# Kernel tuning notes

Measured on AMD Instinct MI355X. Metric: run time of the kernel, lower is better.

## Reference

```python
import jax, jax.numpy as jnp
import numpy as np

B, N, NT, ET = 16, 38, 9, 4
NE = N * (N - 1) // 2          # 703 edge-generation steps
R = N + NE                     # repeat_num = 741 masked subgraphs
H = D = 128                    # nhid / nout
L = 12                         # num_flow_layer
EDIM = ET - 1                  # 3 relation types used by RGCN
EPS = 1e-5
TEMP = 0.1                     # straight-through argmax temperature


def _st_dis(x, w1, b1, w2, b2):
    # MLP -> logits -> straight-through one-hot(argmax)
    h = jnp.tanh(x @ w1.T + b1)
    logits = h @ w2.T + b2
    soft = jax.nn.softmax(logits / TEMP, axis=-1)
    hard = jax.nn.one_hot(jnp.argmax(logits, axis=-1), logits.shape[-1], dtype=logits.dtype)
    return soft + jax.lax.stop_gradient(hard - soft)


def _one_hot_add(inputs, shift):
    # (inputs + shift) mod vocab in one-hot space == circular conv via FFT
    out = jnp.fft.ifft(jnp.fft.fft(inputs, axis=-1) * jnp.fft.fft(shift, axis=-1), axis=-1)
    return jnp.real(out).astype(inputs.dtype)


def _gconv(x, adj, w):
    # x: (b, n, f_in), adj: (b, e, n, n), w: (e*f_out, f_in)
    b, n, _ = x.shape
    s = (x @ w.T).reshape(b, n, EDIM, -1)            # (b, n, e, f_out)
    return jnp.einsum('beij,bjeo->bio', adj, s)      # aggregate over relations


def _rgcn(x, adj, emb_w, gc1_w, gc2_w, gc3_w):
    h = x @ emb_w.T
    h = jax.nn.relu(_gconv(h, adj, gc1_w))
    h = jax.nn.relu(_gconv(h, adj, gc2_w))
    return _gconv(h, adj, gc3_w)                     # no relu on last layer


def setup_inputs():
    key = jax.random.key(0)
    ks = jax.random.split(key, 16)
    s = 0.1
    iu, ju = np.triu_indices(N, k=1)                 # canonical edge order (703, 2)
    return {
        'x': jax.random.uniform(ks[0], (B, N, NT), dtype=jnp.float32),
        'adj': jax.random.uniform(ks[1], (B, ET, N, N), dtype=jnp.float32),
        'x_deq': jax.random.normal(ks[2], (B, N, NT), dtype=jnp.float32),
        'adj_deq': jax.random.normal(ks[3], (B, NE, ET), dtype=jnp.float32),
        'mask_node': jax.random.uniform(ks[4], (R, N)) < 0.5,
        'mask_edge': jax.random.uniform(ks[5], (R, N, N)) < 0.5,
        'index_select_edge': jnp.asarray(np.stack([iu, ju], 1), dtype=jnp.int32),
        'emb_w': jax.random.normal(ks[6], (NT, NT), jnp.float32) * s,
        'gc1_w': jax.random.normal(ks[7], (EDIM * H, NT), jnp.float32) * s,
        'gc2_w': jax.random.normal(ks[8], (EDIM * H, H), jnp.float32) * s,
        'gc3_w': jax.random.normal(ks[9], (EDIM * D, H), jnp.float32) * s,
        'bn_gamma': jnp.ones((D,), jnp.float32),
        'bn_beta': jnp.zeros((D,), jnp.float32),
        'node_w1': jax.random.normal(ks[10], (L, H, D), jnp.float32) * s,
        'node_b1': jnp.zeros((L, H), jnp.float32),
        'node_w2': jax.random.normal(ks[11], (L, NT, H), jnp.float32) * s,
        'node_b2': jnp.zeros((L, NT), jnp.float32),
        'edge_w1': jax.random.normal(ks[12], (L, H, 3 * D), jnp.float32) * s,
        'edge_b1': jnp.zeros((L, H), jnp.float32),
        'edge_w2': jax.random.normal(ks[13], (L, ET, H), jnp.float32) * s,
        'edge_b2': jnp.zeros((L, ET), jnp.float32),
    }


def reference(x, adj, x_deq, adj_deq, mask_node, mask_edge, index_select_edge,
              emb_w, gc1_w, gc2_w, gc3_w, bn_gamma, bn_beta,
              node_w1, node_b1, node_w2, node_b2,
              edge_w1, edge_b1, edge_w2, edge_b2):
    adj3 = adj[:, :EDIM]                                              # (B,3,N,N)
    xr = jnp.where(mask_node[None, :, :, None], x[:, None], 0.0)      # (B,R,N,NT)
    ar = jnp.where(mask_edge[None, :, None], adj3[:, None], 0.0)      # (B,R,3,N,N)
    xr = xr.reshape(B * R, N, NT)
    ar = ar.reshape(B * R, EDIM, N, N)
    node_emb = _rgcn(xr, ar, emb_w, gc1_w, gc2_w, gc3_w)              # (B*R,N,D)
    # BatchNorm1d over channels (training-mode batch statistics, biased var)
    m = node_emb.mean(axis=(0, 1))
    v = node_emb.var(axis=(0, 1))
    node_emb = (node_emb - m) * jax.lax.rsqrt(v + EPS) * bn_gamma + bn_beta
    node_emb = node_emb.reshape(B, R, N, D)
    graph_emb = node_emb.sum(axis=2)                                  # (B,R,D)
    graph_emb_node = graph_emb[:, :N]                                 # (B,N,D)
    graph_emb_edge = graph_emb[:, N:, None]                           # (B,NE,1,D)
    all_node_emb_edge = node_emb[:, N:]                               # (B,NE,N,D)
    idx = jnp.broadcast_to(index_select_edge[None, :, :, None].astype(jnp.int32), (B, NE, 2, D))
    sel = jnp.take_along_axis(all_node_emb_edge, idx, axis=2)         # (B,NE,2,D)
    graph_node_emb_edge = jnp.concatenate([sel, graph_emb_edge], axis=2).reshape(B, NE, 3 * D)
    xd, ad = x_deq, adj_deq
    for i in range(L):
        nt = _st_dis(graph_emb_node, node_w1[i], node_b1[i], node_w2[i], node_b2[i]).astype(x.dtype)
        xd = _one_hot_add(xd, nt)
        et = _st_dis(graph_node_emb_edge, edge_w1[i], edge_b1[i], edge_w2[i], edge_b2[i]).astype(adj.dtype)
        ad = _one_hot_add(ad, et)
    return (xd, ad)
```

## Files before the change

### kernel.cpp

```cpp
#include <hip/hip_runtime.h>

#define B_   16
#define N_   38
#define NT_  9
#define ET_  4
#define NE_  703
#define R_   741
#define L_   12
#define BR_  11856

__global__ __launch_bounds__(128) void k_sx(const float* __restrict__ x,
                                            const float* __restrict__ emb_w,
                                            const float* __restrict__ gc1_w,
                                            float* __restrict__ sx)
{
  int bn = blockIdx.x;
  int t  = threadIdx.x;
  __shared__ float xr[NT_];
  __shared__ float hx[NT_];
  if (t < NT_) xr[t] = x[bn*NT_ + t];
  __syncthreads();
  if (t < NT_) {
    float s = 0.f;
    #pragma unroll
    for (int u = 0; u < NT_; ++u) s += xr[u] * emb_w[t*NT_ + u];
    hx[t] = s;
  }
  __syncthreads();
  for (int eo = t; eo < 384; eo += 128) {
    float s = 0.f;
    #pragma unroll
    for (int u = 0; u < NT_; ++u) s += hx[u] * gc1_w[eo*NT_ + u];
    sx[bn*384 + eo] = s;
  }
}

__global__ __launch_bounds__(128) void k_wt(const float* __restrict__ gc2_w,
                                            const float* __restrict__ gc3_w,
                                            float* __restrict__ Wt)
{
  int blk   = blockIdx.x;
  int which = blk / 384;
  int rem   = blk - which*384;
  int e     = rem >> 7;
  int k     = rem & 127;
  int o     = threadIdx.x;
  const float* src = which ? gc3_w : gc2_w;
  Wt[(((which*3 + e) << 7) + k)*128 + o] = src[((e << 7) + o)*128 + k];
}

__device__ __forceinline__ void fma4(float4& d, float a, const float4& s) {
  d.x += a*s.x; d.y += a*s.y; d.z += a*s.z; d.w += a*s.w;
}

__device__ __forceinline__ void ldA(const float* __restrict__ adj,
                                    const int* __restrict__ mask_edge,
                                    int b, int r, int e, int tid,
                                    float av[5], float a1v[2])
{
  #pragma unroll
  for (int t = 0; t < 5; ++t) {
    int m = tid + (t << 8);
    float v = 0.f;
    if (m < 1216) {
      int j = m >> 5, slot = m & 31;
      int i = (slot >> 2) + ((slot & 3) << 3);
      int   msk = mask_edge[(r*N_ + i)*N_ + j];
      float a   = adj[((b*ET_ + e)*N_ + i)*N_ + j];
      v = msk ? a : 0.f;
    }
    av[t] = v;
  }
  #pragma unroll
  for (int t = 0; t < 2; ++t) {
    int m = tid + (t << 8);
    float v = 0.f;
    if (m < 304) {
      int j = m >> 3;
      int i = (m & 7) + 32;
      if (i < N_) {
        int   msk = mask_edge[(r*N_ + i)*N_ + j];
        float a   = adj[((b*ET_ + e)*N_ + i)*N_ + j];
        v = msk ? a : 0.f;
      }
    }
    a1v[t] = v;
  }
}

__device__ __forceinline__ void stA(float* __restrict__ A4e,
                                    float* __restrict__ A1e, int tid,
                                    const float av[5], const float a1v[2])
{
  #pragma unroll
  for (int t = 0; t < 5; ++t) {
    int m = tid + (t << 8);
    if (m < 1216) A4e[m] = av[t];
  }
  #pragma unroll
  for (int t = 0; t < 2; ++t) {
    int m = tid + (t << 8);
    if (m < 304) A1e[m] = a1v[t];
  }
}

__device__ __forceinline__ void eacc_m(const float* __restrict__ A4e,
                                       const float* __restrict__ A1e,
                                       const float* __restrict__ S_l,
                                       int p, int c,
                                       const int* __restrict__ mn,
                                       float4 d[5])
{
  #pragma unroll 2
  for (int j = 0; j < 38; ++j) {
    if (!mn[j]) continue;
    float4 s4 = *(const float4*)&S_l[(j << 7) + (c << 2)];
    float4 a4 = *(const float4*)&A4e[(j << 5) + (p << 2)];
    float  a1 = A1e[(j << 3) + p];
    fma4(d[0], a4.x, s4); fma4(d[1], a4.y, s4); fma4(d[2], a4.z, s4);
    fma4(d[3], a4.w, s4); fma4(d[4], a1,   s4);
  }
}

__device__ __forceinline__ void eacc_u(const float* __restrict__ A4e,
                                       const float* __restrict__ A1e,
                                       const float* __restrict__ S_l,
                                       int p, int c,
                                       float4 d[5])
{
  #pragma unroll 4
  for (int j = 0; j < 38; ++j) {
    float4 s4 = *(const float4*)&S_l[(j << 7) + (c << 2)];
    float4 a4 = *(const float4*)&A4e[(j << 5) + (p << 2)];
    float  a1 = A1e[(j << 3) + p];
    fma4(d[0], a4.x, s4); fma4(d[1], a4.y, s4); fma4(d[2], a4.z, s4);
    fma4(d[3], a4.w, s4); fma4(d[4], a1,   s4);
  }
}

__device__ __forceinline__ void gemm_fused(const float* __restrict__ H_l,
                                           const float* __restrict__ Wb,
                                           int p, int c, float4 g[3][5])
{
  #pragma unroll
  for (int e = 0; e < 3; ++e)
    #pragma unroll
    for (int q = 0; q < 5; ++q) { g[e][q].x = 0.f; g[e][q].y = 0.f; g[e][q].z = 0.f; g[e][q].w = 0.f; }
  #pragma unroll 1
  for (int k0 = 0; k0 < 128; k0 += 4) {
    float4 h0 = *(const float4*)&H_l[((p+ 0) << 7) + k0];
    float4 h1 = *(const float4*)&H_l[((p+ 8) << 7) + k0];
    float4 h2 = *(const float4*)&H_l[((p+16) << 7) + k0];
    float4 h3 = *(const float4*)&H_l[((p+24) << 7) + k0];
    float4 h4 = *(const float4*)&H_l[((p+32) << 7) + k0];
    #pragma unroll
    for (int e = 0; e < 3; ++e) {
      const float* We = &Wb[(e << 14) + (k0 << 7) + (c << 2)];
      float4 w0 = *(const float4*)&We[  0];
      float4 w1 = *(const float4*)&We[128];
      float4 w2 = *(const float4*)&We[256];
      float4 w3 = *(const float4*)&We[384];
      fma4(g[e][0], h0.x, w0); fma4(g[e][0], h0.y, w1); fma4(g[e][0], h0.z, w2); fma4(g[e][0], h0.w, w3);
      fma4(g[e][1], h1.x, w0); fma4(g[e][1], h1.y, w1); fma4(g[e][1], h1.z, w2); fma4(g[e][1], h1.w, w3);
      fma4(g[e][2], h2.x, w0); fma4(g[e][2], h2.y, w1); fma4(g[e][2], h2.z, w2); fma4(g[e][2], h2.w, w3);
      fma4(g[e][3], h3.x, w0); fma4(g[e][3], h3.y, w1); fma4(g[e][3], h3.z, w2); fma4(g[e][3], h3.w, w3);
      fma4(g[e][4], h4.x, w0); fma4(g[e][4], h4.y, w1); fma4(g[e][4], h4.z, w2); fma4(g[e][4], h4.w, w3);
    }
  }
}

__device__ __forceinline__ void relu_store(float* __restrict__ H_l, int p, int c,
                                           const float4 d[5])
{
  #pragma unroll
  for (int q = 0; q < 5; ++q) {
    float4 t;
    t.x = fmaxf(d[q].x, 0.f); t.y = fmaxf(d[q].y, 0.f);
    t.z = fmaxf(d[q].z, 0.f); t.w = fmaxf(d[q].w, 0.f);
    *(float4*)&H_l[((p + (q << 3)) << 7) + (c << 2)] = t;
  }
}

__global__ __launch_bounds__(256) void k_rgcn(
    const float* __restrict__ adj, const int* __restrict__ mask_node,
    const int* __restrict__ mask_edge, const int* __restrict__ isel,
    const float* __restrict__ sx, const float* __restrict__ Wt,
    float* __restrict__ sumE, float* __restrict__ sumSq,
    float* __restrict__ selw)
{
  const int br  = blockIdx.x;
  const int b   = br / R_;
  const int r   = br - b*R_;
  const int tid = threadIdx.x;
  const int c   = tid & 31;
  const int p   = tid >> 5;

  __shared__ __align__(16) float A4_l[3*1216];
  __shared__ __align__(16) float A1_l[3*304];
  __shared__ __align__(16) float SH_l[40*128];
  __shared__ int mn_l[40];

  if (tid < 40) mn_l[tid] = (tid < 38) ? mask_node[r*N_ + tid] : 0;

  float av[5], a1v[2];
  ldA(adj, mask_edge, b, r, 0, tid, av, a1v);
  __syncthreads();

  float4 d[5];
  #pragma unroll
  for (int q = 0; q < 5; ++q) { d[q].x = d[q].y = d[q].z = d[q].w = 0.f; }

  for (int e = 0; e < 3; ++e) {
    for (int idx = tid; idx < 40*32; idx += 256) {
      int j = idx >> 5, q4 = idx & 31;
      float4 v; v.x = v.y = v.z = v.w = 0.f;
      if (j < N_ && mn_l[j]) v = *(const float4*)&sx[(b*N_ + j)*384 + (e << 7) + (q4 << 2)];
      *(float4*)&SH_l[(j << 7) + (q4 << 2)] = v;
    }
    stA(&A4_l[e*1216], &A1_l[e*304], tid, av, a1v);
    __syncthreads();
    if (e < 2) ldA(adj, mask_edge, b, r, e+1, tid, av, a1v);
    eacc_m(&A4_l[e*1216], &A1_l[e*304], SH_l, p, c, mn_l, d);
    __syncthreads();
  }
  relu_store(SH_l, p, c, d);
  __syncthreads();

  for (int gv = 0; gv < 2; ++gv) {
    float4 g[3][5];
    gemm_fused(SH_l, &Wt[gv*49152], p, c, g);
    #pragma unroll
    for (int q = 0; q < 5; ++q) { d[q].x = d[q].y = d[q].z = d[q].w = 0.f; }
    #pragma unroll
    for (int e = 0; e < 3; ++e) {
      __syncthreads();
      #pragma unroll
      for (int q = 0; q < 5; ++q)
        *(float4*)&SH_l[((p + (q << 3)) << 7) + (c << 2)] = g[e][q];
      __syncthreads();
      eacc_u(&A4_l[e*1216], &A1_l[e*304], SH_l, p, c, d);
    }
    if (gv == 0) {
      __syncthreads();
      relu_store(SH_l, p, c, d);
      __syncthreads();
    }
  }
  __syncthreads();

  {
    float4 sA, sB;
    sA.x = d[0].x+d[1].x+d[2].x+d[3].x+d[4].x;
    sA.y = d[0].y+d[1].y+d[2].y+d[3].y+d[4].y;
    sA.z = d[0].z+d[1].z+d[2].z+d[3].z+d[4].z;
    sA.w = d[0].w+d[1].w+d[2].w+d[3].w+d[4].w;
    sB.x = d[0].x*d[0].x+d[1].x*d[1].x+d[2].x*d[2].x+d[3].x*d[3].x+d[4].x*d[4].x;
    sB.y = d[0].y*d[0].y+d[1].y*d[1].y+d[2].y*d[2].y+d[3].y*d[3].y+d[4].y*d[4].y;
    sB.z = d[0].z*d[0].z+d[1].z*d[1].z+d[2].z*d[2].z+d[3].z*d[3].z+d[4].z*d[4].z;
    sB.w = d[0].w*d[0].w+d[1].w*d[1].w+d[2].w*d[2].w+d[3].w*d[3].w+d[4].w*d[4].w;
    *(float4*)&SH_l[( p      << 7) + (c << 2)] = sA;
    *(float4*)&SH_l[((8 + p) << 7) + (c << 2)] = sB;
  }
  __syncthreads();
  {
    int o = tid & 127, half = tid >> 7;
    float t = 0.f;
    #pragma unroll
    for (int pp = 0; pp < 8; ++pp) t += SH_l[(((half << 3) + pp) << 7) + o];
    if (half == 0) sumE [br*128 + o] = t;
    else           sumSq[br*128 + o] = t;
  }
  if (r >= N_) {
    int k  = r - N_;
    int iu = isel[2*k], ju = isel[2*k+1];
    if (p == (iu & 7)) {
      int mu = iu >> 3;
      float4 v = d[0];
      if (mu == 1) v = d[1]; else if (mu == 2) v = d[2];
      else if (mu == 3) v = d[3]; else if (mu == 4) v = d[4];
      *(float4*)&selw[(((b*NE_ + k)*2 + 0) << 7) + (c << 2)] = v;
    }
    if (p == (ju & 7)) {
      int mu = ju >> 3;
      float4 v = d[0];
      if (mu == 1) v = d[1]; else if (mu == 2) v = d[2];
      else if (mu == 3) v = d[3]; else if (mu == 4) v = d[4];
      *(float4*)&selw[(((b*NE_ + k)*2 + 1) << 7) + (c << 2)] = v;
    }
  }
}

__global__ __launch_bounds__(256) void k_bn1(const float* __restrict__ sumE,
                                             const float* __restrict__ sumSq,
                                             double* __restrict__ part)
{
  int g = blockIdx.x;
  int t = threadIdx.x;
  int o = t & 127, h = t >> 7;
  int lo = g*47;
  int hi = lo + 47; if (hi > BR_) hi = BR_;
  double a1 = 0.0, a2 = 0.0;
  for (int i = lo + h; i < hi; i += 2) {
    a1 += (double)sumE [i*128 + o];
    a2 += (double)sumSq[i*128 + o];
  }
  __shared__ double sh1[256], sh2[256];
  sh1[t] = a1; sh2[t] = a2;
  __syncthreads();
  if (h == 0) {
    part[g*128 + o]           = sh1[o] + sh1[128 + o];
    part[256*128 + g*128 + o] = sh2[o] + sh2[128 + o];
  }
}

__global__ __launch_bounds__(128) void k_bn2(const double* __restrict__ part,
                                             const float* __restrict__ gamma,
                                             const float* __restrict__ beta,
                                             float* __restrict__ bnsc,
                                             float* __restrict__ bnsh)
{
  int o = threadIdx.x;
  double s1 = 0.0, s2 = 0.0;
  for (int g = 0; g < 256; ++g) {
    s1 += part[g*128 + o];
    s2 += part[256*128 + g*128 + o];
  }
  double cnt = (double)BR_ * 38.0;
  double m   = s1 / cnt;
  double var = s2 / cnt - m*m;
  double rs  = 1.0 / sqrt(var + 1e-5);
  double sc  = (double)gamma[o] * rs;
  bnsc[o] = (float)sc;
  bnsh[o] = beta[o] - (float)(m * sc);
}

__global__ __launch_bounds__(128) void k_node(
    const float* __restrict__ sumE, const float* __restrict__ bnsc,
    const float* __restrict__ bnsh,
    const float* __restrict__ w1, const float* __restrict__ b1,
    const float* __restrict__ w2, const float* __restrict__ b2,
    const float* __restrict__ x_deq, float* __restrict__ out)
{
  int blk = blockIdx.x;
  int b   = blk / N_;
  int o   = threadIdx.x;
  __shared__ __align__(16) float xv[128];
  __shared__ __align__(16) float hb[128];
  __shared__ float lg[NT_];
  __shared__ int   P_s;
  int br = b*R_ + (blk - b*N_);
  xv[o] = sumE[br*128 + o]*bnsc[o] + 38.f*bnsh[o];
  if (o == 0) P_s = 0;
  __syncthreads();
  for (int l = 0; l < L_; ++l) {
    const float* wr = &w1[(l*128 + o)*128];
    float s = b1[l*128 + o];
    for (int k = 0; k < 128; k += 4) {
      float4 w4 = *(const float4*)&wr[k];
      s += w4.x*xv[k] + w4.y*xv[k+1] + w4.z*xv[k+2] + w4.w*xv[k+3];
    }
    hb[o] = tanhf(s);
    __syncthreads();
    if (o < NT_) {
      const float* w2r = &w2[(l*NT_ + o)*128];
      float s2 = b2[l*NT_ + o];
      for (int k = 0; k < 128; ++k) s2 += w2r[k]*hb[k];
      lg[o] = s2;
    }
    __syncthreads();
    if (o == 0) {
      int best = 0; float bv = lg[0];
      #pragma unroll
      for (int cc = 1; cc < NT_; ++cc) if (lg[cc] > bv) { bv = lg[cc]; best = cc; }
      P_s += best;
    }
    __syncthreads();
  }
  int P = P_s % NT_;
  if (o < NT_) {
    int srcc = o - P; if (srcc < 0) srcc += NT_;
    out[blk*NT_ + o] = x_deq[blk*NT_ + srcc];
  }
}

__global__ __launch_bounds__(256) void k_edge(
    const float* __restrict__ sumE, const float* __restrict__ selw,
    const float* __restrict__ bnsc, const float* __restrict__ bnsh,
    const float* __restrict__ w1, const float* __restrict__ b1,
    const float* __restrict__ w2, const float* __restrict__ b2,
    const float* __restrict__ adj_deq, float* __restrict__ out)
{
  int k = blockIdx.x;
  int t = threadIdx.x;
  int o = t & 127, g = t >> 7;
  __shared__ __align__(16) float xv[16][384];
  __shared__ __align__(16) float hb[16][132];
  __shared__ float lg[16][4];
  __shared__ int   Pf[16];

  for (int idx = t; idx < 16*128; idx += 256) {
    int b = idx >> 7, oo = idx & 127;
    float sc = bnsc[oo], sh = bnsh[oo];
    int base = ((b*NE_ + k)*2)*128;
    xv[b][oo]       = selw[base + oo]      *sc + sh;
    xv[b][128 + oo] = selw[base + 128 + oo]*sc + sh;
    xv[b][256 + oo] = sumE[(b*R_ + N_ + k)*128 + oo]*sc + 38.f*sh;
  }
  int Preg = 0;
  __syncthreads();

  for (int l = 0; l < L_; ++l) {
    float acc[8];
    #pragma unroll
    for (int bb = 0; bb < 8; ++bb) acc[bb] = b1[l*128 + o];
    const float* wr = &w1[(l*128 + o)*384];
    for (int kk = 0; kk < 384; kk += 4) {
      float4 w4 = *(const float4*)&wr[kk];
      #pragma unroll
      for (int bb = 0; bb < 8; ++bb) {
        float4 h4 = *(const float4*)&xv[g*8 + bb][kk];
        acc[bb] += w4.x*h4.x + w4.y*h4.y + w4.z*h4.z + w4.w*h4.w;
      }
    }
    #pragma unroll
    for (int bb = 0; bb < 8; ++bb) hb[g*8 + bb][o] = tanhf(acc[bb]);
    __syncthreads();
    if (t < 64) {
      int m = t >> 2, c = t & 3;
      const float* w2r = &w2[(l*ET_ + c)*128];
      float s2 = b2[l*ET_ + c];
      for (int kk = 0; kk < 128; ++kk) s2 += w2r[kk]*hb[m][kk];
      lg[m][c] = s2;
    }
    __syncthreads();
    if (t < 16) {
      int best = 0; float bv = lg[t][0];
      #pragma unroll
      for (int c = 1; c < ET_; ++c) if (lg[t][c] > bv) { bv = lg[t][c]; best = c; }
      Preg += best;
    }
    __syncthreads();
  }
  if (t < 16) Pf[t] = Preg & 3;
  __syncthreads();
  if (t < 64) {
    int m = t >> 2, c = t & 3;
    int srcc = c - Pf[m]; if (srcc < 0) srcc += ET_;
    out[(m*NE_ + k)*ET_ + c] = adj_deq[(m*NE_ + k)*ET_ + srcc];
  }
}

extern "C" void kernel_launch(void* const* d_in, const int* in_sizes, int n_in,
                              void* d_out, int out_size, void* d_ws, size_t ws_size,
                              hipStream_t stream)
{
  (void)in_sizes; (void)n_in; (void)out_size; (void)ws_size;

  const float* x         = (const float*)d_in[0];
  const float* adj       = (const float*)d_in[1];
  const float* x_deq     = (const float*)d_in[2];
  const float* adj_deq   = (const float*)d_in[3];
  const int*   mask_node = (const int*)d_in[4];
  const int*   mask_edge = (const int*)d_in[5];
  const int*   isel      = (const int*)d_in[6];
  const float* emb_w     = (const float*)d_in[7];
  const float* gc1_w     = (const float*)d_in[8];
  const float* gc2_w     = (const float*)d_in[9];
  const float* gc3_w     = (const float*)d_in[10];
  const float* bn_gamma  = (const float*)d_in[11];
  const float* bn_beta   = (const float*)d_in[12];
  const float* node_w1   = (const float*)d_in[13];
  const float* node_b1   = (const float*)d_in[14];
  const float* node_w2   = (const float*)d_in[15];
  const float* node_b2   = (const float*)d_in[16];
  const float* edge_w1   = (const float*)d_in[17];
  const float* edge_b1   = (const float*)d_in[18];
  const float* edge_w2   = (const float*)d_in[19];
  const float* edge_b2   = (const float*)d_in[20];

  float* out_f = (float*)d_out;

  float*  wsf   = (float*)d_ws;
  float*  sx    = wsf;
  float*  sumE  = sx    + 233472;
  float*  sumSq = sumE  + 1517568;
  float*  selw  = sumSq + 1517568;
  float*  bnsc  = selw  + 2879488;
  float*  bnsh  = bnsc  + 128;
  double* part  = (double*)(bnsh + 128);
  float*  Wt    = (float*)part;

  k_wt  <<<768,    128, 0, stream>>>(gc2_w, gc3_w, Wt);
  k_sx  <<<B_*N_,  128, 0, stream>>>(x, emb_w, gc1_w, sx);
  k_rgcn<<<BR_,    256, 0, stream>>>(adj, mask_node, mask_edge, isel, sx,
                                     Wt, sumE, sumSq, selw);
  k_bn1 <<<256,    256, 0, stream>>>(sumE, sumSq, part);
  k_bn2 <<<1,      128, 0, stream>>>(part, bn_gamma, bn_beta, bnsc, bnsh);
  k_node<<<B_*N_,  128, 0, stream>>>(sumE, bnsc, bnsh, node_w1, node_b1,
                                     node_w2, node_b2, x_deq, out_f);
  k_edge<<<NE_,    256, 0, stream>>>(sumE, selw, bnsc, bnsh, edge_w1, edge_b1,
                                     edge_w2, edge_b2, adj_deq,
                                     out_f + B_*N_*NT_);
}
```

Before: 2.242 ms.

## Pre-transpose MLP first-layer weights and remap edge-head GEMV thread tiling

Adds a kernel that transposes node_w1 and edge_w1 into k-major layout in the workspace, reusing the sumSq buffer after batch-norm has consumed it. The node and edge head kernels then read weights coalesced across threads instead of each thread striding through its own row. The edge kernel also remaps threads so each computes 4 output channels for 2 batch rows with float4 weight loads, replacing 1 channel for 8 rows. The cost is an extra transpose launch and reliance on sumSq being dead after k_bn1.

```diff
diff --git a/kernel.cpp b/kernel.cpp
--- a/kernel.cpp
+++ b/kernel.cpp
@@ -47,6 +47,23 @@
   int o     = threadIdx.x;
   const float* src = which ? gc3_w : gc2_w;
   Wt[(((which*3 + e) << 7) + k)*128 + o] = src[((e << 7) + o)*128 + k];
+}
+
+__global__ __launch_bounds__(128) void k_wt2(const float* __restrict__ node_w1,
+                                             const float* __restrict__ edge_w1,
+                                             float* __restrict__ w1t_e,
+                                             float* __restrict__ w1t_n)
+{
+  int blk = blockIdx.x;
+  int o   = threadIdx.x;
+  if (blk < 12*384) {
+    int l = blk / 384, kk = blk - l*384;
+    w1t_e[blk*128 + o] = edge_w1[(l*128 + o)*384 + kk];
+  } else {
+    int row = blk - 12*384;
+    int l = row >> 7, k = row & 127;
+    w1t_n[row*128 + o] = node_w1[(l*128 + o)*128 + k];
+  }
 }
 
 __device__ __forceinline__ void fma4(float4& d, float a, const float4& s) {
@@ -337,7 +354,7 @@
 __global__ __launch_bounds__(128) void k_node(
     const float* __restrict__ sumE, const float* __restrict__ bnsc,
     const float* __restrict__ bnsh,
-    const float* __restrict__ w1, const float* __restrict__ b1,
+    const float* __restrict__ w1t_n, const float* __restrict__ b1,
     const float* __restrict__ w2, const float* __restrict__ b2,
     const float* __restrict__ x_deq, float* __restrict__ out)
 {
@@ -353,11 +370,13 @@
   if (o == 0) P_s = 0;
   __syncthreads();
   for (int l = 0; l < L_; ++l) {
-    const float* wr = &w1[(l*128 + o)*128];
+    const float* wb = &w1t_n[(l << 14)];
     float s = b1[l*128 + o];
+    #pragma unroll 2
     for (int k = 0; k < 128; k += 4) {
-      float4 w4 = *(const float4*)&wr[k];
-      s += w4.x*xv[k] + w4.y*xv[k+1] + w4.z*xv[k+2] + w4.w*xv[k+3];
+      float4 x4 = *(const float4*)&xv[k];
+      s += wb[((k+0) << 7) + o]*x4.x + wb[((k+1) << 7) + o]*x4.y
+         + wb[((k+2) << 7) + o]*x4.z + wb[((k+3) << 7) + o]*x4.w;
     }
     hb[o] = tanhf(s);
     __syncthreads();
@@ -386,13 +405,13 @@
 __global__ __launch_bounds__(256) void k_edge(
     const float* __restrict__ sumE, const float* __restrict__ selw,
     const float* __restrict__ bnsc, const float* __restrict__ bnsh,
-    const float* __restrict__ w1, const float* __restrict__ b1,
+    const float* __restrict__ w1t_e, const float* __restrict__ b1,
     const float* __restrict__ w2, const float* __restrict__ b2,
     const float* __restrict__ adj_deq, float* __restrict__ out)
 {
   int k = blockIdx.x;
   int t = threadIdx.x;
-  int o = t & 127, g = t >> 7;
+  int c = t & 31, p = t >> 5;
   __shared__ __align__(16) float xv[16][384];
   __shared__ __align__(16) float hb[16][132];
   __shared__ float lg[16][4];
@@ -410,33 +429,44 @@
   __syncthreads();
 
   for (int l = 0; l < L_; ++l) {
-    float acc[8];
-    #pragma unroll
-    for (int bb = 0; bb < 8; ++bb) acc[bb] = b1[l*128 + o];
-    const float* wr = &w1[(l*128 + o)*384];
+    float4 acc0, acc1;
+    {
+      float4 bb4 = *(const float4*)&b1[(l << 7) + (c << 2)];
+      acc0 = bb4; acc1 = bb4;
+    }
+    const float* wl = &w1t_e[(l*384) << 7];
+    #pragma unroll 2
     for (int kk = 0; kk < 384; kk += 4) {
-      float4 w4 = *(const float4*)&wr[kk];
-      #pragma unroll
-      for (int bb = 0; bb < 8; ++bb) {
-        float4 h4 = *(const float4*)&xv[g*8 + bb][kk];
-        acc[bb] += w4.x*h4.x + w4.y*h4.y + w4.z*h4.z + w4.w*h4.w;
-      }
-    }
-    #pragma unroll
-    for (int bb = 0; bb < 8; ++bb) hb[g*8 + bb][o] = tanhf(acc[bb]);
+      float4 x0 = *(const float4*)&xv[p][kk];
+      float4 x1 = *(const float4*)&xv[p + 8][kk];
+      const float* wk = wl + (kk << 7) + (c << 2);
+      float4 w0 = *(const float4*)&wk[  0];
+      float4 w1 = *(const float4*)&wk[128];
+      float4 w2v= *(const float4*)&wk[256];
+      float4 w3 = *(const float4*)&wk[384];
+      fma4(acc0, x0.x, w0); fma4(acc0, x0.y, w1); fma4(acc0, x0.z, w2v); fma4(acc0, x0.w, w3);
+      fma4(acc1, x1.x, w0); fma4(acc1, x1.y, w1); fma4(acc1, x1.z, w2v); fma4(acc1, x1.w, w3);
+    }
+    {
+      float4 h;
+      h.x = tanhf(acc0.x); h.y = tanhf(acc0.y); h.z = tanhf(acc0.z); h.w = tanhf(acc0.w);
+      *(float4*)&hb[p][c << 2] = h;
+      h.x = tanhf(acc1.x); h.y = tanhf(acc1.y); h.z = tanhf(acc1.z); h.w = tanhf(acc1.w);
+      *(float4*)&hb[p + 8][c << 2] = h;
+    }
     __syncthreads();
     if (t < 64) {
-      int m = t >> 2, c = t & 3;
-      const float* w2r = &w2[(l*ET_ + c)*128];
-      float s2 = b2[l*ET_ + c];
+      int m = t >> 2, c2 = t & 3;
+      const float* w2r = &w2[(l*ET_ + c2)*128];
+      float s2 = b2[l*ET_ + c2];
       for (int kk = 0; kk < 128; ++kk) s2 += w2r[kk]*hb[m][kk];
-      lg[m][c] = s2;
+      lg[m][c2] = s2;
     }
     __syncthreads();
     if (t < 16) {
       int best = 0; float bv = lg[t][0];
       #pragma unroll
-      for (int c = 1; c < ET_; ++c) if (lg[t][c] > bv) { bv = lg[t][c]; best = c; }
+      for (int cc = 1; cc < ET_; ++cc) if (lg[t][cc] > bv) { bv = lg[t][cc]; best = cc; }
       Preg += best;
     }
     __syncthreads();
@@ -444,9 +474,9 @@
   if (t < 16) Pf[t] = Preg & 3;
   __syncthreads();
   if (t < 64) {
-    int m = t >> 2, c = t & 3;
-    int srcc = c - Pf[m]; if (srcc < 0) srcc += ET_;
-    out[(m*NE_ + k)*ET_ + c] = adj_deq[(m*NE_ + k)*ET_ + srcc];
+    int m = t >> 2, c2 = t & 3;
+    int srcc = c2 - Pf[m]; if (srcc < 0) srcc += ET_;
+    out[(m*NE_ + k)*ET_ + c2] = adj_deq[(m*NE_ + k)*ET_ + srcc];
   }
 }
 
@@ -489,16 +519,19 @@
   float*  bnsh  = bnsc  + 128;
   double* part  = (double*)(bnsh + 128);
   float*  Wt    = (float*)part;
-
-  k_wt  <<<768,    128, 0, stream>>>(gc2_w, gc3_w, Wt);
-  k_sx  <<<B_*N_,  128, 0, stream>>>(x, emb_w, gc1_w, sx);
-  k_rgcn<<<BR_,    256, 0, stream>>>(adj, mask_node, mask_edge, isel, sx,
-                                     Wt, sumE, sumSq, selw);
-  k_bn1 <<<256,    256, 0, stream>>>(sumE, sumSq, part);
-  k_bn2 <<<1,      128, 0, stream>>>(part, bn_gamma, bn_beta, bnsc, bnsh);
-  k_node<<<B_*N_,  128, 0, stream>>>(sumE, bnsc, bnsh, node_w1, node_b1,
-                                     node_w2, node_b2, x_deq, out_f);
-  k_edge<<<NE_,    256, 0, stream>>>(sumE, selw, bnsc, bnsh, edge_w1, edge_b1,
-                                     edge_w2, edge_b2, adj_deq,
-                                     out_f + B_*N_*NT_);
-}
+  float*  w1t_e = sumSq;
+  float*  w1t_n = sumSq + 589824;
+
+  k_wt  <<<768,      128, 0, stream>>>(gc2_w, gc3_w, Wt);
+  k_sx  <<<B_*N_,    128, 0, stream>>>(x, emb_w, gc1_w, sx);
+  k_rgcn<<<BR_,      256, 0, stream>>>(adj, mask_node, mask_edge, isel, sx,
+                                       Wt, sumE, sumSq, selw);
+  k_bn1 <<<256,      256, 0, stream>>>(sumE, sumSq, part);
+  k_bn2 <<<1,        128, 0, stream>>>(part, bn_gamma, bn_beta, bnsc, bnsh);
+  k_wt2 <<<12*384 + 12*128, 128, 0, stream>>>(node_w1, edge_w1, w1t_e, w1t_n);
+  k_node<<<B_*N_,    128, 0, stream>>>(sumE, bnsc, bnsh, w1t_n, node_b1,
+                                       node_w2, node_b2, x_deq, out_f);
+  k_edge<<<NE_,      256, 0, stream>>>(sumE, selw, bnsc, bnsh, w1t_e, edge_b1,
+                                       edge_w2, edge_b2, adj_deq,
+                                       out_f + B_*N_*NT_);
+}
```

New measurement: 2.209 ms. Within noise of the previous version (-1.5%).
